# Performance work log

Hardware: AMD Instinct MI355X
Metric: run time of the kernel (lower is better)

Reference implementation:

```python
import jax, jax.numpy as jnp
import numpy as np

KEEP_RATIO = 0.25
BLOCK = 8
TEMP = 0.1


def setup_inputs() -> dict:
    key = jax.random.key(0)
    features = jax.random.normal(key, (8, 256, 132, 132), dtype=jnp.float32)
    return {"features": features, "enabled": 1}


def reference(features, enabled):
    B, C, H, W = features.shape
    if not enabled:
        return jnp.ones((B, C, H, W), dtype=features.dtype)
    # pad H, W up to multiples of BLOCK (zeros, like F.pad default)
    ph = (-H) % BLOCK
    pw = (-W) % BLOCK
    x = jnp.pad(jnp.abs(features), ((0, 0), (0, 0), (0, ph), (0, pw)))
    Hp, Wp = H + ph, W + pw
    nh, nw = Hp // BLOCK, Wp // BLOCK
    # avg_pool2d(kernel=stride=BLOCK) == block-mean via reshape
    pooled = x.reshape(B, C, nh, BLOCK, nw, BLOCK).mean(axis=(3, 5))  # [B,C,nh,nw]
    total = nh * nw
    scores = pooled.reshape(B, C, total)
    keep = max(1, min(total, int(round(total * KEEP_RATIO))))
    top_vals, top_idx = jax.lax.top_k(scores, keep)  # sorted descending, like torch.topk
    # hard mask: scatter ones at topk indices
    flat_idx = top_idx.reshape(B * C, keep)
    hard = (jnp.zeros((B * C, total), dtype=features.dtype)
            .at[jnp.arange(B * C)[:, None], flat_idx].set(1.0)
            .reshape(B, C, total))
    # training-mode straight-through soft blend
    thr = jax.lax.stop_gradient(top_vals[..., -1:])  # kth value as threshold
    soft = jax.nn.sigmoid((scores - thr) / TEMP)
    soft = soft * (keep / jnp.maximum(soft.sum(-1, keepdims=True), 1e-6))
    soft = jnp.clip(soft, 0.0, 1.0)
    mask = jax.lax.stop_gradient(hard) - jax.lax.stop_gradient(soft) + soft
    # upsample blocks back to pixels (repeat_interleave) and crop padding
    block_mask = mask.reshape(B, C, nh, nw)
    full = jnp.repeat(jnp.repeat(block_mask, BLOCK, axis=2), BLOCK, axis=3)
    return full[:, :, :H, :W]
```

## Files before the change

### kernel.cpp

```cpp
#include <hip/hip_runtime.h>


#define HH 132
#define WW 132
#define NB 17
#define TOTAL 289
#define NPAD 320
#define KEEP 72
#define NV ((HH * WW) / 4)
#define PLANES 2048

typedef float floatx4 __attribute__((ext_vector_type(4)));

__global__ __launch_bounds__(NPAD)
void gate_score(const float4* __restrict__ feats4,
                const int* __restrict__ enabled_p,
                unsigned char* __restrict__ ws_mask) {
    const int plane = blockIdx.x;
    const int t = threadIdx.x;
    const float4* __restrict__ fp = feats4 + (size_t)plane * NV;

    __shared__ __align__(16) double   s_score[NPAD];
    __shared__ __align__(16) unsigned s_key[NPAD];

    s_score[t] = 0.0;
    __syncthreads();

    for (int v = t; v < NV; v += NPAD) {
        const float4 x = fp[v];
        const double s = (double)fabsf(x.x) + (double)fabsf(x.y)
                       + (double)fabsf(x.z) + (double)fabsf(x.w);
        const int base = v * 4;
        const int row = base / WW;
        const int col = base - row * WW;
        atomicAdd(&s_score[(row >> 3) * NB + (col >> 3)], s);
    }
    __syncthreads();

    s_key[t] = (unsigned)((unsigned long long)
                   __double_as_longlong(s_score[t]) >> 32);
    __syncthreads();

    const int en = *enabled_p;
    if (t < TOTAL) {
        const unsigned ki = s_key[t];
        const uint4* __restrict__ sk4 = (const uint4*)s_key;
        int r = 0, e = 0;
        #pragma unroll 10
        for (int q = 0; q < NPAD / 4; ++q) {
            const uint4 k = sk4[q];
            r += (int)(k.x > ki) + (int)(k.y > ki)
               + (int)(k.z > ki) + (int)(k.w > ki);
            e += (int)(k.x == ki) + (int)(k.y == ki)
               + (int)(k.z == ki) + (int)(k.w == ki);
        }
        int rank = r;
        if (e > 1) {
            const double si = s_score[t];
            rank = 0;
            for (int j = 0; j < TOTAL; ++j) {
                const double sj = s_score[j];
                rank += (int)((sj > si) || ((sj == si) && (j < t)));
            }
        }
        ws_mask[(size_t)plane * TOTAL + t] =
            (unsigned char)((!en || rank < KEEP) ? 1 : 0);
    }
}

#define NTB 256
__global__ __launch_bounds__(NTB)
void gate_write(const unsigned char* __restrict__ ws_mask,
                float4* __restrict__ out4) {
    const int plane = blockIdx.x;
    const int t = threadIdx.x;
    floatx4* __restrict__ op = (floatx4*)(out4 + (size_t)plane * NV);

    __shared__ float s_hard[TOTAL];
    const unsigned char* __restrict__ mp = ws_mask + (size_t)plane * TOTAL;
    for (int i = t; i < TOTAL; i += NTB) s_hard[i] = (float)mp[i];
    __syncthreads();

    for (int v = t; v < NV; v += NTB) {
        const int base = v * 4;
        const int row = base / WW;
        const int col = base - row * WW;
        const float m = s_hard[(row >> 3) * NB + (col >> 3)];
        const floatx4 mv = {m, m, m, m};
        __builtin_nontemporal_store(mv, &op[v]);
    }
}

__global__ __launch_bounds__(NTB)
void gate_mono(const float4* __restrict__ feats4,
               const int* __restrict__ enabled_p,
               float4* __restrict__ out4) {
    const int plane = blockIdx.x;
    const int t = threadIdx.x;
    const float4* __restrict__ fp = feats4 + (size_t)plane * NV;
    floatx4* __restrict__ op = (floatx4*)(out4 + (size_t)plane * NV);

    __shared__ __align__(16) double   s_score[NPAD];
    __shared__ __align__(16) unsigned s_key[NPAD];
    __shared__ float s_hard[TOTAL];

    for (int i = t; i < NPAD; i += NTB) s_score[i] = 0.0;
    __syncthreads();
    for (int v = t; v < NV; v += NTB) {
        const float4 x = fp[v];
        const double s = (double)fabsf(x.x) + (double)fabsf(x.y)
                       + (double)fabsf(x.z) + (double)fabsf(x.w);
        const int base = v * 4;
        const int row = base / WW;
        const int col = base - row * WW;
        atomicAdd(&s_score[(row >> 3) * NB + (col >> 3)], s);
    }
    __syncthreads();
    for (int i = t; i < NPAD; i += NTB)
        s_key[i] = (unsigned)((unsigned long long)
                       __double_as_longlong(s_score[i]) >> 32);
    __syncthreads();
    const int en = *enabled_p;
    const uint4* __restrict__ sk4 = (const uint4*)s_key;
    for (int i = t; i < TOTAL; i += NTB) {
        const unsigned ki = s_key[i];
        int r = 0, e = 0;
        #pragma unroll 10
        for (int q = 0; q < NPAD / 4; ++q) {
            const uint4 k = sk4[q];
            r += (int)(k.x > ki) + (int)(k.y > ki)
               + (int)(k.z > ki) + (int)(k.w > ki);
            e += (int)(k.x == ki) + (int)(k.y == ki)
               + (int)(k.z == ki) + (int)(k.w == ki);
        }
        int rank = r;
        if (e > 1) {
            const double si = s_score[i];
            rank = 0;
            for (int j = 0; j < TOTAL; ++j) {
                const double sj = s_score[j];
                rank += (int)((sj > si) || ((sj == si) && (j < i)));
            }
        }
        s_hard[i] = (!en || rank < KEEP) ? 1.0f : 0.0f;
    }
    __syncthreads();
    for (int v = t; v < NV; v += NTB) {
        const int base = v * 4;
        const int row = base / WW;
        const int col = base - row * WW;
        const float m = s_hard[(row >> 3) * NB + (col >> 3)];
        const floatx4 mv = {m, m, m, m};
        __builtin_nontemporal_store(mv, &op[v]);
    }
}

extern "C" void kernel_launch(void* const* d_in, const int* in_sizes, int n_in,
                              void* d_out, int out_size, void* d_ws, size_t ws_size,
                              hipStream_t stream) {
    const float4* feats = (const float4*)d_in[0];
    const int* enabled = (const int*)d_in[1];
    float4* out = (float4*)d_out;
    const size_t need = (size_t)PLANES * TOTAL;
    if (d_ws != nullptr && ws_size >= need) {
        unsigned char* mask = (unsigned char*)d_ws;
        gate_score<<<PLANES, NPAD, 0, stream>>>(feats, enabled, mask);
        gate_write<<<PLANES, NTB, 0, stream>>>(mask, out);
    } else {
        gate_mono<<<PLANES, NTB, 0, stream>>>(feats, enabled, out);
    }
}
```

Measured before the change: 278.9 us.

## Split scoring into four blocks per plane and move top-k ranking into write kernel

The scoring kernel now launches four blocks per plane, each owning four or five 8-row strips. Each block stages per-float4 abs sums in shared memory and reduces them deterministically per 8x8 block, replacing the shared-memory double atomics. It writes raw 64-bit score keys to the workspace, and the ranking plus mask construction move into the write kernel. This raises parallelism and removes atomic contention, at the cost of a larger workspace and redundant ranking work in the write stage.

```diff
diff --git a/kernel.cpp b/kernel.cpp
--- a/kernel.cpp
+++ b/kernel.cpp
@@ -7,122 +7,84 @@
 #define TOTAL 289
 #define NPAD 320
 #define KEEP 72
+#define NTH 256
+#define NC4 33
+#define SF4 264
 #define NV ((HH * WW) / 4)
 #define PLANES 2048
 
 typedef float floatx4 __attribute__((ext_vector_type(4)));
 
-__global__ __launch_bounds__(NPAD)
+__global__ __launch_bounds__(NTH)
 void gate_score(const float4* __restrict__ feats4,
-                const int* __restrict__ enabled_p,
-                unsigned char* __restrict__ ws_mask) {
-    const int plane = blockIdx.x;
+                unsigned long long* __restrict__ ws_key) {
+    const int gid = blockIdx.x;
+    const int plane = gid >> 2;
+    const int g = gid & 3;
+    const int sg0 = g * 4;
+    const int ns = (g == 3) ? 5 : 4;
     const int t = threadIdx.x;
     const float4* __restrict__ fp = feats4 + (size_t)plane * NV;
 
-    __shared__ __align__(16) double   s_score[NPAD];
-    __shared__ __align__(16) unsigned s_key[NPAD];
-
-    s_score[t] = 0.0;
-    __syncthreads();
-
-    for (int v = t; v < NV; v += NPAD) {
-        const float4 x = fp[v];
-        const double s = (double)fabsf(x.x) + (double)fabsf(x.y)
-                       + (double)fabsf(x.z) + (double)fabsf(x.w);
-        const int base = v * 4;
-        const int row = base / WW;
-        const int col = base - row * WW;
-        atomicAdd(&s_score[(row >> 3) * NB + (col >> 3)], s);
-    }
-    __syncthreads();
-
-    s_key[t] = (unsigned)((unsigned long long)
-                   __double_as_longlong(s_score[t]) >> 32);
-    __syncthreads();
-
-    const int en = *enabled_p;
-    if (t < TOTAL) {
-        const unsigned ki = s_key[t];
-        const uint4* __restrict__ sk4 = (const uint4*)s_key;
-        int r = 0, e = 0;
-        #pragma unroll 10
-        for (int q = 0; q < NPAD / 4; ++q) {
-            const uint4 k = sk4[q];
-            r += (int)(k.x > ki) + (int)(k.y > ki)
-               + (int)(k.z > ki) + (int)(k.w > ki);
-            e += (int)(k.x == ki) + (int)(k.y == ki)
-               + (int)(k.z == ki) + (int)(k.w == ki);
-        }
-        int rank = r;
-        if (e > 1) {
-            const double si = s_score[t];
-            rank = 0;
-            for (int j = 0; j < TOTAL; ++j) {
-                const double sj = s_score[j];
-                rank += (int)((sj > si) || ((sj == si) && (j < t)));
+    __shared__ __align__(16) double s_e[5 * SF4];
+
+    for (int s = 0; s < ns; ++s) {
+        const int base = (sg0 + s) * SF4;
+        for (int v = t; v < SF4; v += NTH) {
+            const int gi = base + v;
+            double acc = 0.0;
+            if (gi < NV) {
+                const float4 x = fp[gi];
+                acc = (double)fabsf(x.x) + (double)fabsf(x.y)
+                    + (double)fabsf(x.z) + (double)fabsf(x.w);
             }
-        }
-        ws_mask[(size_t)plane * TOTAL + t] =
-            (unsigned char)((!en || rank < KEEP) ? 1 : 0);
-    }
-}
-
-#define NTB 256
-__global__ __launch_bounds__(NTB)
-void gate_write(const unsigned char* __restrict__ ws_mask,
+            s_e[s * SF4 + v] = acc;
+        }
+    }
+    __syncthreads();
+
+    const int nsc = ns * NB;
+    for (int j = t; j < nsc; j += NTH) {
+        const int sl = j / NB;
+        const int i = j - sl * NB;
+        const double* ep = &s_e[sl * SF4];
+        double sum = 0.0;
+        if (i < 16) {
+            #pragma unroll
+            for (int r = 0; r < 8; ++r)
+                sum += ep[r * NC4 + 2 * i] + ep[r * NC4 + 2 * i + 1];
+        } else {
+            #pragma unroll
+            for (int r = 0; r < 8; ++r)
+                sum += ep[r * NC4 + 32];
+        }
+        ws_key[(size_t)plane * NPAD + (sg0 + sl) * NB + i] =
+            (unsigned long long)__double_as_longlong(sum);
+    }
+}
+
+__global__ __launch_bounds__(NTH)
+void gate_write(const unsigned long long* __restrict__ ws_key,
+                const int* __restrict__ enabled_p,
                 float4* __restrict__ out4) {
     const int plane = blockIdx.x;
     const int t = threadIdx.x;
-    floatx4* __restrict__ op = (floatx4*)(out4 + (size_t)plane * NV);
-
-    __shared__ float s_hard[TOTAL];
-    const unsigned char* __restrict__ mp = ws_mask + (size_t)plane * TOTAL;
-    for (int i = t; i < TOTAL; i += NTB) s_hard[i] = (float)mp[i];
-    __syncthreads();
-
-    for (int v = t; v < NV; v += NTB) {
-        const int base = v * 4;
-        const int row = base / WW;
-        const int col = base - row * WW;
-        const float m = s_hard[(row >> 3) * NB + (col >> 3)];
-        const floatx4 mv = {m, m, m, m};
-        __builtin_nontemporal_store(mv, &op[v]);
-    }
-}
-
-__global__ __launch_bounds__(NTB)
-void gate_mono(const float4* __restrict__ feats4,
-               const int* __restrict__ enabled_p,
-               float4* __restrict__ out4) {
-    const int plane = blockIdx.x;
-    const int t = threadIdx.x;
-    const float4* __restrict__ fp = feats4 + (size_t)plane * NV;
-    floatx4* __restrict__ op = (floatx4*)(out4 + (size_t)plane * NV);
-
-    __shared__ __align__(16) double   s_score[NPAD];
+
+    __shared__ __align__(16) unsigned long long s_k64[NPAD];
     __shared__ __align__(16) unsigned s_key[NPAD];
     __shared__ float s_hard[TOTAL];
 
-    for (int i = t; i < NPAD; i += NTB) s_score[i] = 0.0;
-    __syncthreads();
-    for (int v = t; v < NV; v += NTB) {
-        const float4 x = fp[v];
-        const double s = (double)fabsf(x.x) + (double)fabsf(x.y)
-                       + (double)fabsf(x.z) + (double)fabsf(x.w);
-        const int base = v * 4;
-        const int row = base / WW;
-        const int col = base - row * WW;
-        atomicAdd(&s_score[(row >> 3) * NB + (col >> 3)], s);
-    }
-    __syncthreads();
-    for (int i = t; i < NPAD; i += NTB)
-        s_key[i] = (unsigned)((unsigned long long)
-                       __double_as_longlong(s_score[i]) >> 32);
-    __syncthreads();
+    const unsigned long long* __restrict__ kp = ws_key + (size_t)plane * NPAD;
+    for (int i = t; i < NPAD; i += NTH) {
+        const unsigned long long k = (i < TOTAL) ? kp[i] : 0ULL;
+        s_k64[i] = k;
+        s_key[i] = (unsigned)(k >> 32);
+    }
+    __syncthreads();
+
     const int en = *enabled_p;
     const uint4* __restrict__ sk4 = (const uint4*)s_key;
-    for (int i = t; i < TOTAL; i += NTB) {
+    for (int i = t; i < TOTAL; i += NTH) {
         const unsigned ki = s_key[i];
         int r = 0, e = 0;
         #pragma unroll 10
@@ -135,6 +97,72 @@
         }
         int rank = r;
         if (e > 1) {
+            const unsigned long long ki64 = s_k64[i];
+            rank = 0;
+            for (int j = 0; j < TOTAL; ++j) {
+                const unsigned long long kj = s_k64[j];
+                rank += (int)((kj > ki64) || ((kj == ki64) && (j < i)));
+            }
+        }
+        s_hard[i] = (!en || rank < KEEP) ? 1.0f : 0.0f;
+    }
+    __syncthreads();
+
+    floatx4* __restrict__ op = (floatx4*)(out4 + (size_t)plane * NV);
+    for (int v = t; v < NV; v += NTH) {
+        const int base = v * 4;
+        const int row = base / WW;
+        const int col = base - row * WW;
+        const float m = s_hard[(row >> 3) * NB + (col >> 3)];
+        const floatx4 mv = {m, m, m, m};
+        __builtin_nontemporal_store(mv, &op[v]);
+    }
+}
+
+__global__ __launch_bounds__(NTH)
+void gate_mono(const float4* __restrict__ feats4,
+               const int* __restrict__ enabled_p,
+               float4* __restrict__ out4) {
+    const int plane = blockIdx.x;
+    const int t = threadIdx.x;
+    const float4* __restrict__ fp = feats4 + (size_t)plane * NV;
+    floatx4* __restrict__ op = (floatx4*)(out4 + (size_t)plane * NV);
+
+    __shared__ __align__(16) double   s_score[NPAD];
+    __shared__ __align__(16) unsigned s_key[NPAD];
+    __shared__ float s_hard[TOTAL];
+
+    for (int i = t; i < NPAD; i += NTH) s_score[i] = 0.0;
+    __syncthreads();
+    for (int v = t; v < NV; v += NTH) {
+        const float4 x = fp[v];
+        const double s = (double)fabsf(x.x) + (double)fabsf(x.y)
+                       + (double)fabsf(x.z) + (double)fabsf(x.w);
+        const int base = v * 4;
+        const int row = base / WW;
+        const int col = base - row * WW;
+        atomicAdd(&s_score[(row >> 3) * NB + (col >> 3)], s);
+    }
+    __syncthreads();
+    for (int i = t; i < NPAD; i += NTH)
+        s_key[i] = (unsigned)((unsigned long long)
+                       __double_as_longlong(s_score[i]) >> 32);
+    __syncthreads();
+    const int en = *enabled_p;
+    const uint4* __restrict__ sk4 = (const uint4*)s_key;
+    for (int i = t; i < TOTAL; i += NTH) {
+        const unsigned ki = s_key[i];
+        int r = 0, e = 0;
+        #pragma unroll 10
+        for (int q = 0; q < NPAD / 4; ++q) {
+            const uint4 k = sk4[q];
+            r += (int)(k.x > ki) + (int)(k.y > ki)
+               + (int)(k.z > ki) + (int)(k.w > ki);
+            e += (int)(k.x == ki) + (int)(k.y == ki)
+               + (int)(k.z == ki) + (int)(k.w == ki);
+        }
+        int rank = r;
+        if (e > 1) {
             const double si = s_score[i];
             rank = 0;
             for (int j = 0; j < TOTAL; ++j) {
@@ -145,7 +173,7 @@
         s_hard[i] = (!en || rank < KEEP) ? 1.0f : 0.0f;
     }
     __syncthreads();
-    for (int v = t; v < NV; v += NTB) {
+    for (int v = t; v < NV; v += NTH) {
         const int base = v * 4;
         const int row = base / WW;
         const int col = base - row * WW;
@@ -161,12 +189,12 @@
     const float4* feats = (const float4*)d_in[0];
     const int* enabled = (const int*)d_in[1];
     float4* out = (float4*)d_out;
-    const size_t need = (size_t)PLANES * TOTAL;
+    const size_t need = (size_t)PLANES * NPAD * sizeof(unsigned long long);
     if (d_ws != nullptr && ws_size >= need) {
-        unsigned char* mask = (unsigned char*)d_ws;
-        gate_score<<<PLANES, NPAD, 0, stream>>>(feats, enabled, mask);
-        gate_write<<<PLANES, NTB, 0, stream>>>(mask, out);
+        unsigned long long* wkey = (unsigned long long*)d_ws;
+        gate_score<<<PLANES * 4, NTH, 0, stream>>>(feats, wkey);
+        gate_write<<<PLANES, NTH, 0, stream>>>(wkey, enabled, out);
     } else {
-        gate_mono<<<PLANES, NTB, 0, stream>>>(feats, enabled, out);
-    }
-}
+        gate_mono<<<PLANES, NTH, 0, stream>>>(feats, enabled, out);
+    }
+}
```

Measured after the change: 273.2 us. 1.02x faster.
